# Performance work log

Measured on AMD Instinct MI355X. Metric: run time of the kernel, lower is better.

Reference implementation:

```python
import jax, jax.numpy as jnp
import numpy as np

N_NODES = 100000
N_EDGES = 1600000
IN_DIM = 128
OUT_DIM = 64


def setup_inputs() -> dict:
    key = jax.random.key(0)
    k1, k2, k3, k4, k5 = jax.random.split(key, 5)
    x = jax.random.normal(k1, (N_NODES, IN_DIM), dtype=jnp.float32)
    src = jax.random.randint(k2, (N_EDGES,), 0, N_NODES)
    dst = jax.random.randint(k3, (N_EDGES,), 0, N_NODES)
    edge_index = jnp.stack([src, dst]).astype(jnp.int64)
    # Glorot-ish init scale for the two GCN weight matrices (bias=False)
    W1 = jax.random.normal(k4, (IN_DIM, OUT_DIM), dtype=jnp.float32) / np.sqrt(IN_DIM)
    W2 = jax.random.normal(k5, (OUT_DIM, OUT_DIM), dtype=jnp.float32) / np.sqrt(OUT_DIM)
    return {"x": x, "edge_index": edge_index, "W1": W1, "W2": W2}


def _gcn_conv(h, W, src, dst, dinv_sqrt, n_nodes):
    """PyG GCNConv (bias=False): out[i] = sum_{j->i} d_j^-1/2 d_i^-1/2 (h_j @ W),
    with self-loops already folded into (src, dst, dinv_sqrt)."""
    h = h @ W                                    # [N, out]
    norm = dinv_sqrt[src] * dinv_sqrt[dst]       # [E+N]
    msg = h[src] * norm[:, None]                 # gather + scale, [E+N, out]
    return jax.ops.segment_sum(msg, dst, num_segments=n_nodes)


def reference(x, edge_index, W1, W2):
    n = x.shape[0]
    # add self-loops (static shape: E + N edges)
    loop = jnp.arange(n, dtype=edge_index.dtype)
    src = jnp.concatenate([edge_index[0], loop])
    dst = jnp.concatenate([edge_index[1], loop])
    # symmetric normalization degrees (in-degree over dst, unit edge weights)
    deg = jax.ops.segment_sum(jnp.ones_like(dst, dtype=x.dtype), dst, num_segments=n)
    dinv_sqrt = jax.lax.rsqrt(deg)  # deg >= 1 because of self-loops
    # dropout is identity in eval mode (training=False)
    h = _gcn_conv(x, W1, src, dst, dinv_sqrt, n)
    h = jax.nn.relu(h)
    out = _gcn_conv(h, W2, src, dst, dinv_sqrt, n)
    return out
```

## Files before the change

### kernel.cpp

```cpp
#include <hip/hip_runtime.h>
#include <hip/hip_bf16.h>

#define IN_DIM  128
#define OUT_DIM 64
#define EPB 4096
#define NBK_MAX 512

typedef short  bf16x8 __attribute__((ext_vector_type(8)));
typedef float  f32x4  __attribute__((ext_vector_type(4)));

__device__ __forceinline__ unsigned short f2bf(float f) {
    unsigned u = __float_as_uint(f);
    u += 0x7fffu + ((u >> 16) & 1u);
    return (unsigned short)(u >> 16);
}
__device__ __forceinline__ float bf2f(unsigned short h) {
    return __uint_as_float((unsigned)h << 16);
}


__global__ __launch_bounds__(256) void k_cnt(const int* __restrict__ dst,
                                             unsigned* __restrict__ colcnt,
                                             int nE, int nbk, int nblk) {
    __shared__ unsigned h[NBK_MAX];
    for (int b = threadIdx.x; b < NBK_MAX; b += 256) h[b] = 0u;
    __syncthreads();
    int blk = blockIdx.x;
    int e0 = blk * EPB, e1 = min(e0 + EPB, nE);
    for (int e = e0 + threadIdx.x; e < e1; e += 256)
        atomicAdd(&h[dst[e] >> 8], 1u);
    __syncthreads();
    for (int b = threadIdx.x; b < nbk; b += 256)
        colcnt[(size_t)b * nblk + blk] = h[b];
}

__global__ __launch_bounds__(512) void k_bsum(unsigned* __restrict__ colcnt,
                                              unsigned* __restrict__ btot,
                                              int nbk, int nblk) {
    __shared__ unsigned s[512];
    int b = blockIdx.x;
    unsigned v = (threadIdx.x < (unsigned)nblk) ? colcnt[(size_t)b * nblk + threadIdx.x] : 0u;
    s[threadIdx.x] = v;
    __syncthreads();
    for (int d = 1; d < 512; d <<= 1) {
        unsigned t = (threadIdx.x >= (unsigned)d) ? s[threadIdx.x - d] : 0u;
        __syncthreads();
        s[threadIdx.x] += t;
        __syncthreads();
    }
    if (threadIdx.x < (unsigned)nblk)
        colcnt[(size_t)b * nblk + threadIdx.x] = s[threadIdx.x] - v;
    if (threadIdx.x == 511) btot[b] = s[511];
}

__global__ __launch_bounds__(512) void k_btots(const unsigned* __restrict__ btot,
                                               unsigned* __restrict__ bbase,
                                               int nbk, int nE) {
    __shared__ unsigned s[512];
    unsigned v = (threadIdx.x < (unsigned)nbk) ? btot[threadIdx.x] : 0u;
    s[threadIdx.x] = v;
    __syncthreads();
    for (int d = 1; d < 512; d <<= 1) {
        unsigned t = (threadIdx.x >= (unsigned)d) ? s[threadIdx.x - d] : 0u;
        __syncthreads();
        s[threadIdx.x] += t;
        __syncthreads();
    }
    if (threadIdx.x < (unsigned)nbk) bbase[threadIdx.x] = s[threadIdx.x] - v;
    if (threadIdx.x == 0) bbase[nbk] = (unsigned)nE;
}

__global__ __launch_bounds__(256) void k_part(const int* __restrict__ src,
                                              const int* __restrict__ dst,
                                              const unsigned* __restrict__ colcnt,
                                              const unsigned* __restrict__ bbase,
                                              unsigned* __restrict__ ebuf,
                                              int nE, int nbk, int nblk) {
    __shared__ unsigned curs[NBK_MAX];
    int blk = blockIdx.x;
    for (int b = threadIdx.x; b < nbk; b += 256)
        curs[b] = bbase[b] + colcnt[(size_t)b * nblk + blk];
    __syncthreads();
    int e0 = blk * EPB, e1 = min(e0 + EPB, nE);
    for (int e = e0 + threadIdx.x; e < e1; e += 256) {
        int d = dst[e], s = src[e];
        unsigned p = atomicAdd(&curs[d >> 8], 1u);
        ebuf[p] = ((unsigned)(d & 255) << 17) | (unsigned)s;
    }
}

__global__ __launch_bounds__(256) void k_fine(const unsigned* __restrict__ ebuf,
                                              const unsigned* __restrict__ bbase,
                                              unsigned* __restrict__ offs,
                                              float* __restrict__ dinv,
                                              int* __restrict__ perm, int n) {
    __shared__ unsigned deg[256], pos[256], cur[256];
    int b = blockIdx.x;
    int node0 = b << 8;
    unsigned ebeg = bbase[b], eend = bbase[b + 1];
    deg[threadIdx.x] = 0u;
    __syncthreads();
    for (unsigned e = ebeg + threadIdx.x; e < eend; e += 256)
        atomicAdd(&deg[ebuf[e] >> 17], 1u);
    __syncthreads();
    unsigned v = deg[threadIdx.x];
    pos[threadIdx.x] = v;
    __syncthreads();
    for (int d = 1; d < 256; d <<= 1) {
        unsigned t = (threadIdx.x >= (unsigned)d) ? pos[threadIdx.x - d] : 0u;
        __syncthreads();
        pos[threadIdx.x] += t;
        __syncthreads();
    }
    unsigned excl = pos[threadIdx.x] - v;
    cur[threadIdx.x] = excl;
    int node = node0 + threadIdx.x;
    if (node < n) {
        offs[node] = ebeg + excl;
        dinv[node] = rsqrtf((float)v + 1.0f);
    }
    __syncthreads();
    for (unsigned e = ebeg + threadIdx.x; e < eend; e += 256) {
        unsigned rec = ebuf[e];
        unsigned p = atomicAdd(&cur[rec >> 17], 1u);
        perm[ebeg + p] = (int)(rec & 0x1FFFFu);
    }
}

template <int KD, bool RELU>
__global__ __launch_bounds__(256) void k_linm(const float* __restrict__ in,
                                              const float* __restrict__ W,
                                              const float* __restrict__ dinv,
                                              unsigned short* __restrict__ outp, int n) {
    constexpr int LDK = KD + 8;
    __shared__ unsigned short WH[64 * LDK];
    __shared__ unsigned short WL[64 * LDK];
    for (int i = threadIdx.x; i < KD * 64; i += 256) {
        int k = i >> 6, c = i & 63;
        float wv = W[i];
        unsigned short h = f2bf(wv);
        WH[c * LDK + k] = h;
        WL[c * LDK + k] = f2bf(wv - bf2f(h));
    }
    __syncthreads();

    int wid = threadIdx.x >> 6, lane = threadIdx.x & 63;
    int r0 = blockIdx.x * 64 + wid * 16;

    constexpr int NK = KD / 32;
    int arow = r0 + (lane & 15);
    int ar = arow < n ? arow : (n - 1);
    int k8 = (lane >> 4) * 8;

    bf16x8 ah[NK], al[NK];
    {
        const float* rp = in + (size_t)ar * KD;
        float dvin = RELU ? dinv[ar] : 0.f;
#pragma unroll
        for (int ks = 0; ks < NK; ++ks) {
            float4 v0 = *(const float4*)(rp + ks * 32 + k8);
            float4 v1 = *(const float4*)(rp + ks * 32 + k8 + 4);
            float xv[8] = {v0.x, v0.y, v0.z, v0.w, v1.x, v1.y, v1.z, v1.w};
#pragma unroll
            for (int j = 0; j < 8; ++j) {
                float f = xv[j];
                if (RELU) f = fmaxf(dvin * f, 0.f);
                unsigned short h = f2bf(f);
                ah[ks][j] = (short)h;
                al[ks][j] = (short)f2bf(f - bf2f(h));
            }
        }
    }

    f32x4 acc[4];
#pragma unroll
    for (int nt = 0; nt < 4; ++nt) {
        int col = nt * 16 + (lane & 15);
        const unsigned short* bh = &WH[col * LDK + k8];
        const unsigned short* bl = &WL[col * LDK + k8];
        f32x4 a = {0.f, 0.f, 0.f, 0.f};
#pragma unroll
        for (int ks = 0; ks < NK; ++ks) {
            bf16x8 Bh = *(const bf16x8*)(bh + ks * 32);
            bf16x8 Bl = *(const bf16x8*)(bl + ks * 32);
            a = __builtin_amdgcn_mfma_f32_16x16x32_bf16(ah[ks], Bh, a, 0, 0, 0);
            a = __builtin_amdgcn_mfma_f32_16x16x32_bf16(ah[ks], Bl, a, 0, 0, 0);
            a = __builtin_amdgcn_mfma_f32_16x16x32_bf16(al[ks], Bh, a, 0, 0, 0);
        }
        acc[nt] = a;
    }

    int orow0 = r0 + (lane >> 4) * 4;
#pragma unroll
    for (int j = 0; j < 4; ++j) {
        int row = orow0 + j;
        if (row < n) {
            float dv = dinv[row];
#pragma unroll
            for (int nt = 0; nt < 4; ++nt)
                outp[(size_t)row * 64 + nt * 16 + (lane & 15)] = f2bf(dv * acc[nt][j]);
        }
    }
}

template <bool FIN>
__global__ __launch_bounds__(256) void k_gather(const unsigned short* __restrict__ hs,
                                                const unsigned* __restrict__ offs,
                                                const int* __restrict__ perm,
                                                const float* __restrict__ dinv,
                                                float* __restrict__ outb,
                                                int n, int nE) {
    int lane = threadIdx.x & 63;
    int g = lane >> 4, li = lane & 15;
    int base = (blockIdx.x * 4 + (threadIdx.x >> 6)) * 8;
    int rA = base + g;
    int rB = base + 4 + g;
    bool vA = rA < n, vB = rB < n;
    int rcA = vA ? rA : (n - 1);
    int rcB = vB ? rB : (n - 1);
    unsigned begA = offs[rcA];
    unsigned endA = (rcA + 1 < n) ? offs[rcA + 1] : (unsigned)nE;
    unsigned begB = offs[rcB];
    unsigned endB = (rcB + 1 < n) ? offs[rcB + 1] : (unsigned)nE;
    unsigned degA = vA ? (endA - begA) : 0u;
    unsigned degB = vB ? (endB - begB) : 0u;

    float4 qA0, qA1 = {0.f,0.f,0.f,0.f}, qA2 = qA1, qA3 = qA1;
    float4 qB0, qB1 = qA1, qB2 = qA1, qB3 = qA1;
    {
        ushort4 sv = *(const ushort4*)(hs + (size_t)rcA * 64 + li * 4);
        qA0.x = bf2f(sv.x); qA0.y = bf2f(sv.y); qA0.z = bf2f(sv.z); qA0.w = bf2f(sv.w);
        ushort4 tv = *(const ushort4*)(hs + (size_t)rcB * 64 + li * 4);
        qB0.x = bf2f(tv.x); qB0.y = bf2f(tv.y); qB0.z = bf2f(tv.z); qB0.w = bf2f(tv.w);
    }

    unsigned dm = max(degA, degB);
    dm = max(dm, (unsigned)__shfl_xor((int)dm, 16));
    dm = max(dm, (unsigned)__shfl_xor((int)dm, 32));

    int slA = (li < (int)degA) ? perm[begA + li] : 0;
    int slB = (li < (int)degB) ? perm[begB + li] : 0;

    for (unsigned c0 = 0; c0 < dm; c0 += 16) {
        int sAc = slA, sBc = slB;
        unsigned c1 = c0 + 16;
        if (c1 < dm) {
            slA = (c1 + li < degA) ? perm[begA + c1 + li] : 0;
            slB = (c1 + li < degB) ? perm[begB + c1 + li] : 0;
        }
#pragma unroll
        for (int k = 0; k < 16; ++k) {
            int sA = __shfl(sAc, g * 16 + k);
            int sB = __shfl(sBc, g * 16 + k);
            if (c0 + k < degA) {
                ushort4 v = *(const ushort4*)(hs + (size_t)sA * 64 + li * 4);
                float4* q = (k & 2) ? ((k & 1) ? &qA3 : &qA2) : ((k & 1) ? &qA1 : &qA0);
                q->x += bf2f(v.x); q->y += bf2f(v.y); q->z += bf2f(v.z); q->w += bf2f(v.w);
            }
            if (c0 + k < degB) {
                ushort4 v = *(const ushort4*)(hs + (size_t)sB * 64 + li * 4);
                float4* q = (k & 2) ? ((k & 1) ? &qB3 : &qB2) : ((k & 1) ? &qB1 : &qB0);
                q->x += bf2f(v.x); q->y += bf2f(v.y); q->z += bf2f(v.z); q->w += bf2f(v.w);
            }
        }
    }

    if (vA) {
        float4 acc;
        acc.x = (qA0.x + qA1.x) + (qA2.x + qA3.x);
        acc.y = (qA0.y + qA1.y) + (qA2.y + qA3.y);
        acc.z = (qA0.z + qA1.z) + (qA2.z + qA3.z);
        acc.w = (qA0.w + qA1.w) + (qA2.w + qA3.w);
        if (FIN) {
            float dv = dinv[rA];
            acc.x *= dv; acc.y *= dv; acc.z *= dv; acc.w *= dv;
        }
        *(float4*)(outb + (size_t)rA * 64 + li * 4) = acc;
    }
    if (vB) {
        float4 acc;
        acc.x = (qB0.x + qB1.x) + (qB2.x + qB3.x);
        acc.y = (qB0.y + qB1.y) + (qB2.y + qB3.y);
        acc.z = (qB0.z + qB1.z) + (qB2.z + qB3.z);
        acc.w = (qB0.w + qB1.w) + (qB2.w + qB3.w);
        if (FIN) {
            float dv = dinv[rB];
            acc.x *= dv; acc.y *= dv; acc.z *= dv; acc.w *= dv;
        }
        *(float4*)(outb + (size_t)rB * 64 + li * 4) = acc;
    }
}

extern "C" void kernel_launch(void* const* d_in, const int* in_sizes, int n_in,
                              void* d_out, int out_size, void* d_ws, size_t ws_size,
                              hipStream_t stream) {
    const float* x  = (const float*)d_in[0];
    const int*   ei = (const int*)d_in[1];
    const float* W1 = (const float*)d_in[2];
    const float* W2 = (const float*)d_in[3];
    float* out = (float*)d_out;

    int n  = in_sizes[0] / IN_DIM;
    int nE = in_sizes[1] / 2;
    const int* src = ei;
    const int* dst = ei + nE;

    int nbk  = (n + 255) >> 8;
    int nblk = (nE + EPB - 1) / EPB;

    char* w = (char*)d_ws;
    size_t nAl = ((size_t)n * 4 + 255) & ~(size_t)255;
    float*          dinv   = (float*)w;     w += nAl;
    unsigned*       offs   = (unsigned*)w;  w += nAl;
    unsigned*       colcnt = (unsigned*)w;  w += ((size_t)nbk * nblk * 4 + 255) & ~(size_t)255;
    unsigned*       btot   = (unsigned*)w;  w += ((size_t)nbk * 4 + 255) & ~(size_t)255;
    unsigned*       bbase  = (unsigned*)w;  w += ((size_t)(nbk + 1) * 4 + 255) & ~(size_t)255;
    unsigned*       ebuf   = (unsigned*)w;  w += ((size_t)nE * 4 + 255) & ~(size_t)255;
    int*            perm   = (int*)w;       w += ((size_t)nE * 4 + 255) & ~(size_t)255;
    unsigned short* hs     = (unsigned short*)w; w += (size_t)n * 64 * 2;
    float*          agg    = out;

    int gRow = (n + 31) / 32;
    int gMf  = (n + 63) / 64;

    k_cnt  <<<nblk, 256, 0, stream>>>(dst, colcnt, nE, nbk, nblk);
    k_bsum <<<nbk,  512, 0, stream>>>(colcnt, btot, nbk, nblk);
    k_btots<<<1,    512, 0, stream>>>(btot, bbase, nbk, nE);
    k_part <<<nblk, 256, 0, stream>>>(src, dst, colcnt, bbase, ebuf, nE, nbk, nblk);
    k_fine <<<nbk,  256, 0, stream>>>(ebuf, bbase, offs, dinv, perm, n);

    k_linm<IN_DIM, false><<<gMf, 256, 0, stream>>>(x, W1, dinv, hs, n);
    k_gather<false><<<gRow, 256, 0, stream>>>(hs, offs, perm, dinv, agg, n, nE);

    k_linm<OUT_DIM, true><<<gMf, 256, 0, stream>>>(agg, W2, dinv, hs, n);
    k_gather<true><<<gRow, 256, 0, stream>>>(hs, offs, perm, dinv, out, n, nE);
}
```

Before: 169.1 us.

## Fuse layer-1 gather with ReLU and layer-2 linear transform into one kernel

The first-layer neighbor aggregation, normalization, ReLU and the second-layer 64x64 matmul now run in one kernel. Each block aggregates 32 rows into LDS as split bf16 hi/lo and runs MFMA against W2 to write bf16 hs2 directly. This removes the fp32 write and re-read of the intermediate aggregate plus one kernel launch. In exchange, every block re-converts W2 into shared memory and uses more LDS per block, which can lower occupancy for the latency-bound gather.

```diff
diff --git a/kernel.cpp b/kernel.cpp
--- a/kernel.cpp
+++ b/kernel.cpp
@@ -17,7 +17,6 @@
 __device__ __forceinline__ float bf2f(unsigned short h) {
     return __uint_as_float((unsigned)h << 16);
 }
-
 
 __global__ __launch_bounds__(256) void k_cnt(const int* __restrict__ dst,
                                              unsigned* __restrict__ colcnt,
@@ -127,7 +126,7 @@
     }
 }
 
-template <int KD, bool RELU>
+template <int KD>
 __global__ __launch_bounds__(256) void k_linm(const float* __restrict__ in,
                                               const float* __restrict__ W,
                                               const float* __restrict__ dinv,
@@ -155,7 +154,6 @@
     bf16x8 ah[NK], al[NK];
     {
         const float* rp = in + (size_t)ar * KD;
-        float dvin = RELU ? dinv[ar] : 0.f;
 #pragma unroll
         for (int ks = 0; ks < NK; ++ks) {
             float4 v0 = *(const float4*)(rp + ks * 32 + k8);
@@ -164,7 +162,6 @@
 #pragma unroll
             for (int j = 0; j < 8; ++j) {
                 float f = xv[j];
-                if (RELU) f = fmaxf(dvin * f, 0.f);
                 unsigned short h = f2bf(f);
                 ah[ks][j] = (short)h;
                 al[ks][j] = (short)f2bf(f - bf2f(h));
@@ -203,13 +200,155 @@
     }
 }
 
-template <bool FIN>
-__global__ __launch_bounds__(256) void k_gather(const unsigned short* __restrict__ hs,
-                                                const unsigned* __restrict__ offs,
-                                                const int* __restrict__ perm,
-                                                const float* __restrict__ dinv,
-                                                float* __restrict__ outb,
-                                                int n, int nE) {
+__global__ __launch_bounds__(256) void k_gl(const unsigned short* __restrict__ hs,
+                                            const unsigned* __restrict__ offs,
+                                            const int* __restrict__ perm,
+                                            const float* __restrict__ dinv,
+                                            const float* __restrict__ W2,
+                                            unsigned short* __restrict__ hs2,
+                                            int n, int nE) {
+    constexpr int LDK = 72;
+    __shared__ unsigned short WH[64 * LDK];
+    __shared__ unsigned short WL[64 * LDK];
+    __shared__ unsigned short AH[32 * LDK];
+    __shared__ unsigned short AL[32 * LDK];
+
+    for (int i = threadIdx.x; i < 64 * 64; i += 256) {
+        int k = i >> 6, c = i & 63;
+        float wv = W2[i];
+        unsigned short h = f2bf(wv);
+        WH[c * LDK + k] = h;
+        WL[c * LDK + k] = f2bf(wv - bf2f(h));
+    }
+
+    int lane = threadIdx.x & 63;
+    int wv_ = threadIdx.x >> 6;
+    int g = lane >> 4, li = lane & 15;
+    int base = blockIdx.x * 32;
+    int lA = wv_ * 8 + g, lB = lA + 4;
+    int rA = base + lA, rB = base + lB;
+    bool vA = rA < n, vB = rB < n;
+    int rcA = vA ? rA : (n - 1);
+    int rcB = vB ? rB : (n - 1);
+    unsigned begA = offs[rcA];
+    unsigned endA = (rcA + 1 < n) ? offs[rcA + 1] : (unsigned)nE;
+    unsigned begB = offs[rcB];
+    unsigned endB = (rcB + 1 < n) ? offs[rcB + 1] : (unsigned)nE;
+    unsigned degA = vA ? (endA - begA) : 0u;
+    unsigned degB = vB ? (endB - begB) : 0u;
+
+    float4 qA0, qA1 = {0.f,0.f,0.f,0.f}, qA2 = qA1, qA3 = qA1;
+    float4 qB0, qB1 = qA1, qB2 = qA1, qB3 = qA1;
+    {
+        ushort4 sv = *(const ushort4*)(hs + (size_t)rcA * 64 + li * 4);
+        qA0.x = bf2f(sv.x); qA0.y = bf2f(sv.y); qA0.z = bf2f(sv.z); qA0.w = bf2f(sv.w);
+        ushort4 tv = *(const ushort4*)(hs + (size_t)rcB * 64 + li * 4);
+        qB0.x = bf2f(tv.x); qB0.y = bf2f(tv.y); qB0.z = bf2f(tv.z); qB0.w = bf2f(tv.w);
+    }
+
+    unsigned dm = max(degA, degB);
+    dm = max(dm, (unsigned)__shfl_xor((int)dm, 16));
+    dm = max(dm, (unsigned)__shfl_xor((int)dm, 32));
+
+    int slA = (li < (int)degA) ? perm[begA + li] : 0;
+    int slB = (li < (int)degB) ? perm[begB + li] : 0;
+
+    for (unsigned c0 = 0; c0 < dm; c0 += 16) {
+        int sAc = slA, sBc = slB;
+        unsigned c1 = c0 + 16;
+        if (c1 < dm) {
+            slA = (c1 + li < degA) ? perm[begA + c1 + li] : 0;
+            slB = (c1 + li < degB) ? perm[begB + c1 + li] : 0;
+        }
+#pragma unroll
+        for (int k = 0; k < 16; ++k) {
+            int sA = __shfl(sAc, g * 16 + k);
+            int sB = __shfl(sBc, g * 16 + k);
+            if (c0 + k < degA) {
+                ushort4 v = *(const ushort4*)(hs + (size_t)sA * 64 + li * 4);
+                float4* q = (k & 2) ? ((k & 1) ? &qA3 : &qA2) : ((k & 1) ? &qA1 : &qA0);
+                q->x += bf2f(v.x); q->y += bf2f(v.y); q->z += bf2f(v.z); q->w += bf2f(v.w);
+            }
+            if (c0 + k < degB) {
+                ushort4 v = *(const ushort4*)(hs + (size_t)sB * 64 + li * 4);
+                float4* q = (k & 2) ? ((k & 1) ? &qB3 : &qB2) : ((k & 1) ? &qB1 : &qB0);
+                q->x += bf2f(v.x); q->y += bf2f(v.y); q->z += bf2f(v.z); q->w += bf2f(v.w);
+            }
+        }
+    }
+
+    {
+        float dvA = dinv[rcA], dvB = dinv[rcB];
+        float4 aA, aB;
+        aA.x = (qA0.x + qA1.x) + (qA2.x + qA3.x);
+        aA.y = (qA0.y + qA1.y) + (qA2.y + qA3.y);
+        aA.z = (qA0.z + qA1.z) + (qA2.z + qA3.z);
+        aA.w = (qA0.w + qA1.w) + (qA2.w + qA3.w);
+        aB.x = (qB0.x + qB1.x) + (qB2.x + qB3.x);
+        aB.y = (qB0.y + qB1.y) + (qB2.y + qB3.y);
+        aB.z = (qB0.z + qB1.z) + (qB2.z + qB3.z);
+        aB.w = (qB0.w + qB1.w) + (qB2.w + qB3.w);
+        float fA[4] = {fmaxf(dvA * aA.x, 0.f), fmaxf(dvA * aA.y, 0.f),
+                       fmaxf(dvA * aA.z, 0.f), fmaxf(dvA * aA.w, 0.f)};
+        float fB[4] = {fmaxf(dvB * aB.x, 0.f), fmaxf(dvB * aB.y, 0.f),
+                       fmaxf(dvB * aB.z, 0.f), fmaxf(dvB * aB.w, 0.f)};
+        ushort4 hA, lA4, hB, lB4;
+        hA.x = f2bf(fA[0]); lA4.x = f2bf(fA[0] - bf2f(hA.x));
+        hA.y = f2bf(fA[1]); lA4.y = f2bf(fA[1] - bf2f(hA.y));
+        hA.z = f2bf(fA[2]); lA4.z = f2bf(fA[2] - bf2f(hA.z));
+        hA.w = f2bf(fA[3]); lA4.w = f2bf(fA[3] - bf2f(hA.w));
+        hB.x = f2bf(fB[0]); lB4.x = f2bf(fB[0] - bf2f(hB.x));
+        hB.y = f2bf(fB[1]); lB4.y = f2bf(fB[1] - bf2f(hB.y));
+        hB.z = f2bf(fB[2]); lB4.z = f2bf(fB[2] - bf2f(hB.z));
+        hB.w = f2bf(fB[3]); lB4.w = f2bf(fB[3] - bf2f(hB.w));
+        *(ushort4*)&AH[lA * LDK + li * 4] = hA;
+        *(ushort4*)&AL[lA * LDK + li * 4] = lA4;
+        *(ushort4*)&AH[lB * LDK + li * 4] = hB;
+        *(ushort4*)&AL[lB * LDK + li * 4] = lB4;
+    }
+    __syncthreads();
+
+    int stripe = wv_ >> 1;
+    int ntb = (wv_ & 1) * 2;
+    int arow = stripe * 16 + (lane & 15);
+    int k8 = (lane >> 4) * 8;
+    bf16x8 ah[2], al[2];
+#pragma unroll
+    for (int ks = 0; ks < 2; ++ks) {
+        ah[ks] = *(const bf16x8*)&AH[arow * LDK + ks * 32 + k8];
+        al[ks] = *(const bf16x8*)&AL[arow * LDK + ks * 32 + k8];
+    }
+#pragma unroll
+    for (int t = 0; t < 2; ++t) {
+        int nt = ntb + t;
+        int col = nt * 16 + (lane & 15);
+        const unsigned short* bh = &WH[col * LDK + k8];
+        const unsigned short* bl = &WL[col * LDK + k8];
+        f32x4 a = {0.f, 0.f, 0.f, 0.f};
+#pragma unroll
+        for (int ks = 0; ks < 2; ++ks) {
+            bf16x8 Bh = *(const bf16x8*)(bh + ks * 32);
+            bf16x8 Bl = *(const bf16x8*)(bl + ks * 32);
+            a = __builtin_amdgcn_mfma_f32_16x16x32_bf16(ah[ks], Bh, a, 0, 0, 0);
+            a = __builtin_amdgcn_mfma_f32_16x16x32_bf16(ah[ks], Bl, a, 0, 0, 0);
+            a = __builtin_amdgcn_mfma_f32_16x16x32_bf16(al[ks], Bh, a, 0, 0, 0);
+        }
+        int orow0 = base + stripe * 16 + (lane >> 4) * 4;
+#pragma unroll
+        for (int j = 0; j < 4; ++j) {
+            int row = orow0 + j;
+            if (row < n)
+                hs2[(size_t)row * 64 + col] = f2bf(dinv[row] * a[j]);
+        }
+    }
+}
+
+__global__ __launch_bounds__(256) void k_gather2(const unsigned short* __restrict__ hs,
+                                                 const unsigned* __restrict__ offs,
+                                                 const int* __restrict__ perm,
+                                                 const float* __restrict__ dinv,
+                                                 float* __restrict__ outb,
+                                                 int n, int nE) {
     int lane = threadIdx.x & 63;
     int g = lane >> 4, li = lane & 15;
     int base = (blockIdx.x * 4 + (threadIdx.x >> 6)) * 8;
@@ -271,10 +410,8 @@
         acc.y = (qA0.y + qA1.y) + (qA2.y + qA3.y);
         acc.z = (qA0.z + qA1.z) + (qA2.z + qA3.z);
         acc.w = (qA0.w + qA1.w) + (qA2.w + qA3.w);
-        if (FIN) {
-            float dv = dinv[rA];
-            acc.x *= dv; acc.y *= dv; acc.z *= dv; acc.w *= dv;
-        }
+        float dv = dinv[rA];
+        acc.x *= dv; acc.y *= dv; acc.z *= dv; acc.w *= dv;
         *(float4*)(outb + (size_t)rA * 64 + li * 4) = acc;
     }
     if (vB) {
@@ -283,10 +420,8 @@
         acc.y = (qB0.y + qB1.y) + (qB2.y + qB3.y);
         acc.z = (qB0.z + qB1.z) + (qB2.z + qB3.z);
         acc.w = (qB0.w + qB1.w) + (qB2.w + qB3.w);
-        if (FIN) {
-            float dv = dinv[rB];
-            acc.x *= dv; acc.y *= dv; acc.z *= dv; acc.w *= dv;
-        }
+        float dv = dinv[rB];
+        acc.x *= dv; acc.y *= dv; acc.z *= dv; acc.w *= dv;
         *(float4*)(outb + (size_t)rB * 64 + li * 4) = acc;
     }
 }
@@ -318,10 +453,10 @@
     unsigned*       ebuf   = (unsigned*)w;  w += ((size_t)nE * 4 + 255) & ~(size_t)255;
     int*            perm   = (int*)w;       w += ((size_t)nE * 4 + 255) & ~(size_t)255;
     unsigned short* hs     = (unsigned short*)w; w += (size_t)n * 64 * 2;
-    float*          agg    = out;
-
-    int gRow = (n + 31) / 32;
+    unsigned short* hs2    = (unsigned short*)w; w += (size_t)n * 64 * 2;
+
     int gMf  = (n + 63) / 64;
+    int gFus = (n + 31) / 32;
 
     k_cnt  <<<nblk, 256, 0, stream>>>(dst, colcnt, nE, nbk, nblk);
     k_bsum <<<nbk,  512, 0, stream>>>(colcnt, btot, nbk, nblk);
@@ -329,9 +464,9 @@
     k_part <<<nblk, 256, 0, stream>>>(src, dst, colcnt, bbase, ebuf, nE, nbk, nblk);
     k_fine <<<nbk,  256, 0, stream>>>(ebuf, bbase, offs, dinv, perm, n);
 
-    k_linm<IN_DIM, false><<<gMf, 256, 0, stream>>>(x, W1, dinv, hs, n);
-    k_gather<false><<<gRow, 256, 0, stream>>>(hs, offs, perm, dinv, agg, n, nE);
-
-    k_linm<OUT_DIM, true><<<gMf, 256, 0, stream>>>(agg, W2, dinv, hs, n);
-    k_gather<true><<<gRow, 256, 0, stream>>>(hs, offs, perm, dinv, out, n, nE);
-}
+    k_linm<IN_DIM><<<gMf, 256, 0, stream>>>(x, W1, dinv, hs, n);
+
+    k_gl<<<gFus, 256, 0, stream>>>(hs, offs, perm, dinv, W2, hs2, n, nE);
+
+    k_gather2<<<(n + 31) / 32, 256, 0, stream>>>(hs2, offs, perm, dinv, out, n, nE);
+}
```

New measurement: 180.0 us. 6.4% more time.
